# Kernel tuning notes

Measured on AMD Instinct MI355X. Metric: run time of the kernel, lower is better.

Reference implementation:

```python
import jax, jax.numpy as jnp
import numpy as np

VOCAB = 50257
D_EMB = 1024
N_NODES = 4096

def setup_inputs() -> dict:
    key = jax.random.key(0)
    k1, k2, k3 = jax.random.split(key, 3)
    x = jax.random.normal(k1, (N_NODES, D_EMB), dtype=jnp.float32)
    W = jax.random.normal(k2, (VOCAB, D_EMB), dtype=jnp.float32) * 0.02
    y = jax.random.randint(k3, (N_NODES,), 0, VOCAB, dtype=jnp.int64)
    return {"x": x, "W": W, "y": y}

def reference(x, W, y):
    # Decoder: logits = x @ W.T  -> (n_nodes, vocab)
    logits = jnp.einsum('nd,vd->nv', x, W)
    # CrossEntropyLoss (mean reduction)
    logp = jax.nn.log_softmax(logits, axis=-1)
    nll = -jnp.take_along_axis(logp, y[:, None], axis=-1)[:, 0]
    return jnp.mean(nll)
```

## Files before the change

### kernel.cpp

```cpp
#include <hip/hip_runtime.h>
#include <hip/hip_bf16.h>
#include <math.h>


#define N_NODES 4096
#define D_EMB   1024
#define VOCAB   50257
#define VPAD    50304
#define NT      393

typedef __attribute__((ext_vector_type(8))) short short8;
typedef __attribute__((ext_vector_type(4))) float f32x4;

__device__ __forceinline__ unsigned short f2bf(float f) {
  unsigned int x = __float_as_uint(f);
  x += 0x7fffu + ((x >> 16) & 1u);
  return (unsigned short)(x >> 16);
}

__global__ void cvt_w_kernel(const float* __restrict__ W, unsigned short* __restrict__ Wb) {
  long long gid = (long long)blockIdx.x * 256 + threadIdx.x;
  long long e = gid << 3;
  int row = (int)(e >> 10);
  short8 o;
  if (row < VOCAB) {
    const float4* p = (const float4*)(W + e);
    float4 u = p[0];
    float4 v = p[1];
    o[0] = (short)f2bf(u.x); o[1] = (short)f2bf(u.y); o[2] = (short)f2bf(u.z); o[3] = (short)f2bf(u.w);
    o[4] = (short)f2bf(v.x); o[5] = (short)f2bf(v.y); o[6] = (short)f2bf(v.z); o[7] = (short)f2bf(v.w);
  } else {
    o[0]=0; o[1]=0; o[2]=0; o[3]=0; o[4]=0; o[5]=0; o[6]=0; o[7]=0;
  }
  *(short8*)(Wb + e) = o;
}

__global__ void cvt_x_kernel(const float* __restrict__ x, unsigned short* __restrict__ Xb) {
  long long gid = (long long)blockIdx.x * 256 + threadIdx.x;
  long long e = gid << 3;
  const float4* p = (const float4*)(x + e);
  float4 u = p[0];
  float4 v = p[1];
  short8 o;
  o[0] = (short)f2bf(u.x); o[1] = (short)f2bf(u.y); o[2] = (short)f2bf(u.z); o[3] = (short)f2bf(u.w);
  o[4] = (short)f2bf(v.x); o[5] = (short)f2bf(v.y); o[6] = (short)f2bf(v.z); o[7] = (short)f2bf(v.w);
  *(short8*)(Xb + e) = o;
}

__global__ void dot_y_kernel(const float* __restrict__ x, const float* __restrict__ W,
                             const int* __restrict__ y, float* __restrict__ logit_y) {
  __shared__ float red[4];
  const int n = blockIdx.x;
  const int t = threadIdx.x;
  const int lbl = y[n];
  const float* xr = x + ((long long)n << 10);
  const float* wr = W + ((long long)lbl << 10);
  float s = 0.f;
  #pragma unroll
  for (int i = 0; i < 4; ++i) {
    int k = t + i * 256;
    s = fmaf(xr[k], wr[k], s);
  }
  #pragma unroll
  for (int m = 32; m; m >>= 1) s += __shfl_xor(s, m, 64);
  if ((t & 63) == 0) red[t >> 6] = s;
  __syncthreads();
  if (t == 0) logit_y[n] = red[0] + red[1] + red[2] + red[3];
}

__global__ __launch_bounds__(256) void gemm_stats_kernel(
    const unsigned short* __restrict__ Xb,
    const unsigned short* __restrict__ Wb,
    float2* __restrict__ partials)
{
  __shared__ unsigned short As[128 * 64];
  __shared__ unsigned short Bs[128 * 64];
  __shared__ float2 stats[128][2];

  const int tid  = threadIdx.x;
  const int lane = tid & 63;
  const int wid  = tid >> 6;
  const int wr   = wid >> 1;
  const int wc   = wid & 1;
  const int g    = lane >> 4;
  const int r16  = lane & 15;

  const int rowTile = blockIdx.x;
  const int vocTile = blockIdx.y;

  const long long abase = (long long)rowTile * 128 * D_EMB;
  const long long bbase = (long long)vocTile * 128 * D_EMB;

  f32x4 acc[4][4];
  #pragma unroll
  for (int m = 0; m < 4; ++m)
    #pragma unroll
    for (int n = 0; n < 4; ++n)
      #pragma unroll
      for (int j = 0; j < 4; ++j)
        acc[m][n][j] = 0.f;

  const int kk_st  = (tid & 7) << 3;
  const int row_st = tid >> 3;

  for (int k0 = 0; k0 < D_EMB; k0 += 64) {
    if (k0) __syncthreads();
    #pragma unroll
    for (int it = 0; it < 4; ++it) {
      const int idx = it * 256 + tid;
      const int row = it * 32 + row_st;
      const unsigned short* ga = Xb + abase + (long long)row * D_EMB + k0 + kk_st;
      const unsigned short* gb = Wb + bbase + (long long)row * D_EMB + k0 + kk_st;
      __builtin_amdgcn_global_load_lds((const __attribute__((address_space(1))) void*)ga,
                                       (__attribute__((address_space(3))) void*)(As + idx * 8),
                                       16, 0, 0);
      __builtin_amdgcn_global_load_lds((const __attribute__((address_space(1))) void*)gb,
                                       (__attribute__((address_space(3))) void*)(Bs + idx * 8),
                                       16, 0, 0);
    }
    __syncthreads();

    short8 a[4][2], b[4][2];
    #pragma unroll
    for (int m = 0; m < 4; ++m)
      #pragma unroll
      for (int kk = 0; kk < 2; ++kk)
        a[m][kk] = *(const short8*)(As + (wr * 64 + m * 16 + r16) * 64 + kk * 32 + g * 8);
    #pragma unroll
    for (int n = 0; n < 4; ++n)
      #pragma unroll
      for (int kk = 0; kk < 2; ++kk)
        b[n][kk] = *(const short8*)(Bs + (wc * 64 + n * 16 + r16) * 64 + kk * 32 + g * 8);

    #pragma unroll
    for (int m = 0; m < 4; ++m)
      #pragma unroll
      for (int n = 0; n < 4; ++n) {
        acc[m][n] = __builtin_amdgcn_mfma_f32_16x16x32_bf16(a[m][0], b[n][0], acc[m][n], 0, 0, 0);
        acc[m][n] = __builtin_amdgcn_mfma_f32_16x16x32_bf16(a[m][1], b[n][1], acc[m][n], 0, 0, 0);
      }
  }

  const int colbase = vocTile * 128 + wc * 64;
  #pragma unroll
  for (int m = 0; m < 4; ++m) {
    #pragma unroll
    for (int j = 0; j < 4; ++j) {
      float vmax = -INFINITY;
      #pragma unroll
      for (int n = 0; n < 4; ++n) {
        const int colg = colbase + n * 16 + r16;
        float v = (colg < VOCAB) ? acc[m][n][j] : -INFINITY;
        vmax = fmaxf(vmax, v);
      }
      vmax = fmaxf(vmax, __shfl_xor(vmax, 1));
      vmax = fmaxf(vmax, __shfl_xor(vmax, 2));
      vmax = fmaxf(vmax, __shfl_xor(vmax, 4));
      vmax = fmaxf(vmax, __shfl_xor(vmax, 8));
      float ssum = 0.f;
      #pragma unroll
      for (int n = 0; n < 4; ++n) {
        const int colg = colbase + n * 16 + r16;
        if (colg < VOCAB) ssum += __expf(acc[m][n][j] - vmax);
      }
      ssum += __shfl_xor(ssum, 1);
      ssum += __shfl_xor(ssum, 2);
      ssum += __shfl_xor(ssum, 4);
      ssum += __shfl_xor(ssum, 8);
      if (r16 == 0) {
        const int rloc = wr * 64 + m * 16 + g * 4 + j;
        stats[rloc][wc] = make_float2(vmax, ssum);
      }
    }
  }
  __syncthreads();
  if (tid < 128) {
    float2 p0 = stats[tid][0];
    float2 p1 = stats[tid][1];
    float M = fmaxf(p0.x, p1.x);
    float S = p0.y * __expf(p0.x - M) + p1.y * __expf(p1.x - M);
    partials[(long long)vocTile * N_NODES + rowTile * 128 + tid] = make_float2(M, S);
  }
}

__global__ void lse_kernel(const float2* __restrict__ partials,
                           const float* __restrict__ logit_y,
                           float* __restrict__ row_nll) {
  const int n = blockIdx.x * 256 + threadIdx.x;
  float M = -INFINITY, S = 0.f;
  for (int t = 0; t < NT; ++t) {
    float2 p = partials[(long long)t * N_NODES + n];
    float newM = fmaxf(M, p.x);
    S = S * __expf(M - newM) + p.y * __expf(p.x - newM);
    M = newM;
  }
  row_nll[n] = (M + logf(S)) - logit_y[n];
}

__global__ void mean_kernel(const float* __restrict__ row_nll, float* __restrict__ out) {
  __shared__ float red[4];
  float s = 0.f;
  for (int i = threadIdx.x; i < N_NODES; i += 256) s += row_nll[i];
  #pragma unroll
  for (int m = 32; m; m >>= 1) s += __shfl_xor(s, m, 64);
  if ((threadIdx.x & 63) == 0) red[threadIdx.x >> 6] = s;
  __syncthreads();
  if (threadIdx.x == 0) out[0] = (red[0] + red[1] + red[2] + red[3]) * (1.0f / N_NODES);
}

extern "C" void kernel_launch(void* const* d_in, const int* in_sizes, int n_in,
                              void* d_out, int out_size, void* d_ws, size_t ws_size,
                              hipStream_t stream) {
  const float* x = (const float*)d_in[0];
  const float* W = (const float*)d_in[1];
  const int*   y = (const int*)d_in[2];
  float* out = (float*)d_out;

  char* ws = (char*)d_ws;
  unsigned short* Wb = (unsigned short*)ws;
  unsigned short* Xb = (unsigned short*)(ws + 103022592);
  float2* partials   = (float2*)(ws + 111411200);
  float* logit_y     = (float*)(ws + 124289024);
  float* row_nll     = (float*)(ws + 124305408);

  hipLaunchKernelGGL(cvt_w_kernel, dim3(VPAD * (D_EMB / 8) / 256), dim3(256), 0, stream, W, Wb);
  hipLaunchKernelGGL(cvt_x_kernel, dim3(N_NODES * (D_EMB / 8) / 256), dim3(256), 0, stream, x, Xb);
  hipLaunchKernelGGL(dot_y_kernel, dim3(N_NODES), dim3(256), 0, stream, x, W, y, logit_y);
  hipLaunchKernelGGL(gemm_stats_kernel, dim3(32, NT), dim3(256), 0, stream, Xb, Wb, partials);
  hipLaunchKernelGGL(lse_kernel, dim3(N_NODES / 256), dim3(256), 0, stream, partials, logit_y, row_nll);
  hipLaunchKernelGGL(mean_kernel, dim3(1), dim3(256), 0, stream, row_nll, out);
}
```

Before: 964.2 us.

## Use 256x256 double-buffered swizzled GEMM tiles with prefetch and row-major partials

Replaces the 128x128 single-buffered GEMM with a 256x256 tile per 512-thread block. LDS is double-buffered so the next k-slice is prefetched during MFMA work, and the LDS layout is XOR-swizzled to avoid bank conflicts. MFMA sections run at raised wave priority. Partials are stored row-major so the LSE kernel can reduce each row with a full wavefront. The larger tile cuts global reloads of X and W, but it raises register and LDS pressure and adds more padding.

```diff
diff --git a/kernel.cpp b/kernel.cpp
--- a/kernel.cpp
+++ b/kernel.cpp
@@ -6,8 +6,9 @@
 #define N_NODES 4096
 #define D_EMB   1024
 #define VOCAB   50257
-#define VPAD    50304
-#define NT      393
+#define VPAD    50432
+#define NT      197
+#define KT      16
 
 typedef __attribute__((ext_vector_type(8))) short short8;
 typedef __attribute__((ext_vector_type(4))) float f32x4;
@@ -68,89 +69,162 @@
   if (t == 0) logit_y[n] = red[0] + red[1] + red[2] + red[3];
 }
 
-__global__ __launch_bounds__(256) void gemm_stats_kernel(
+#define MFMAQ(Q, AF)                                                                  \
+  do {                                                                                \
+    _Pragma("unroll")                                                                 \
+    for (int ni = 0; ni < 4; ++ni) {                                                  \
+      _Pragma("unroll")                                                               \
+      for (int kk = 0; kk < 2; ++kk) {                                                \
+        acc[2*(Q)  ][ni] = __builtin_amdgcn_mfma_f32_16x16x32_bf16(AF[0][kk], bf[ni][kk], acc[2*(Q)  ][ni], 0, 0, 0); \
+        acc[2*(Q)+1][ni] = __builtin_amdgcn_mfma_f32_16x16x32_bf16(AF[1][kk], bf[ni][kk], acc[2*(Q)+1][ni], 0, 0, 0); \
+      }                                                                               \
+    }                                                                                 \
+  } while (0)
+
+#define STAGE(U)                                                                      \
+  do {                                                                                \
+    const int _b = (U) & 1;                                                           \
+    const long long _ko = (long long)(U) * 64;                                        \
+    _Pragma("unroll")                                                                 \
+    for (int h = 0; h < 2; ++h) {                                                     \
+      _Pragma("unroll")                                                               \
+      for (int p = 0; p < 2; ++p) {                                                   \
+        __builtin_amdgcn_global_load_lds(                                             \
+            (const __attribute__((address_space(1))) void*)(Xb + abase[h][p] + _ko),  \
+            (__attribute__((address_space(3))) void*)(sh + _b*32768 + h*8192 + p*4096 + dst0), \
+            16, 0, 0);                                                                \
+      }                                                                               \
+    }                                                                                 \
+    _Pragma("unroll")                                                                 \
+    for (int h = 0; h < 2; ++h) {                                                     \
+      _Pragma("unroll")                                                               \
+      for (int p = 0; p < 2; ++p) {                                                   \
+        __builtin_amdgcn_global_load_lds(                                             \
+            (const __attribute__((address_space(1))) void*)(Wb + bbase[h][p] + _ko),  \
+            (__attribute__((address_space(3))) void*)(sh + _b*32768 + 16384 + h*8192 + p*4096 + dst0), \
+            16, 0, 0);                                                                \
+      }                                                                               \
+    }                                                                                 \
+  } while (0)
+
+__global__ __launch_bounds__(512, 2) void gemm_stats_kernel(
     const unsigned short* __restrict__ Xb,
     const unsigned short* __restrict__ Wb,
     float2* __restrict__ partials)
 {
-  __shared__ unsigned short As[128 * 64];
-  __shared__ unsigned short Bs[128 * 64];
-  __shared__ float2 stats[128][2];
+  __shared__ __align__(16) unsigned short sh[65536];
 
   const int tid  = threadIdx.x;
   const int lane = tid & 63;
   const int wid  = tid >> 6;
-  const int wr   = wid >> 1;
-  const int wc   = wid & 1;
+  const int wr   = wid >> 2;
+  const int wcol = wid & 3;
   const int g    = lane >> 4;
   const int r16  = lane & 15;
 
-  const int rowTile = blockIdx.x;
-  const int vocTile = blockIdx.y;
-
-  const long long abase = (long long)rowTile * 128 * D_EMB;
-  const long long bbase = (long long)vocTile * 128 * D_EMB;
-
-  f32x4 acc[4][4];
-  #pragma unroll
-  for (int m = 0; m < 4; ++m)
+  const int bm0 = blockIdx.x * 256;
+  const int bn0 = blockIdx.y * 256;
+
+  const int srb = tid >> 3;
+  const int scg = ((tid & 7) << 3) ^ ((srb & 7) << 3);
+  const int dst0 = tid * 8;
+  long long abase[2][2], bbase[2][2];
+  #pragma unroll
+  for (int h = 0; h < 2; ++h)
+    #pragma unroll
+    for (int p = 0; p < 2; ++p) {
+      abase[h][p] = (long long)(bm0 + h*128 + p*64 + srb) * D_EMB + scg;
+      bbase[h][p] = (long long)(bn0 + h*128 + p*64 + srb) * D_EMB + scg;
+    }
+
+  f32x4 acc[8][4];
+  #pragma unroll
+  for (int m = 0; m < 8; ++m)
     #pragma unroll
     for (int n = 0; n < 4; ++n)
       #pragma unroll
       for (int j = 0; j < 4; ++j)
         acc[m][n][j] = 0.f;
 
-  const int kk_st  = (tid & 7) << 3;
-  const int row_st = tid >> 3;
-
-  for (int k0 = 0; k0 < D_EMB; k0 += 64) {
-    if (k0) __syncthreads();
-    #pragma unroll
-    for (int it = 0; it < 4; ++it) {
-      const int idx = it * 256 + tid;
-      const int row = it * 32 + row_st;
-      const unsigned short* ga = Xb + abase + (long long)row * D_EMB + k0 + kk_st;
-      const unsigned short* gb = Wb + bbase + (long long)row * D_EMB + k0 + kk_st;
-      __builtin_amdgcn_global_load_lds((const __attribute__((address_space(1))) void*)ga,
-                                       (__attribute__((address_space(3))) void*)(As + idx * 8),
-                                       16, 0, 0);
-      __builtin_amdgcn_global_load_lds((const __attribute__((address_space(1))) void*)gb,
-                                       (__attribute__((address_space(3))) void*)(Bs + idx * 8),
-                                       16, 0, 0);
-    }
-    __syncthreads();
-
-    short8 a[4][2], b[4][2];
-    #pragma unroll
-    for (int m = 0; m < 4; ++m)
-      #pragma unroll
-      for (int kk = 0; kk < 2; ++kk)
-        a[m][kk] = *(const short8*)(As + (wr * 64 + m * 16 + r16) * 64 + kk * 32 + g * 8);
-    #pragma unroll
-    for (int n = 0; n < 4; ++n)
-      #pragma unroll
-      for (int kk = 0; kk < 2; ++kk)
-        b[n][kk] = *(const short8*)(Bs + (wc * 64 + n * 16 + r16) * 64 + kk * 32 + g * 8);
-
-    #pragma unroll
-    for (int m = 0; m < 4; ++m)
-      #pragma unroll
-      for (int n = 0; n < 4; ++n) {
-        acc[m][n] = __builtin_amdgcn_mfma_f32_16x16x32_bf16(a[m][0], b[n][0], acc[m][n], 0, 0, 0);
-        acc[m][n] = __builtin_amdgcn_mfma_f32_16x16x32_bf16(a[m][1], b[n][1], acc[m][n], 0, 0, 0);
-      }
-  }
-
-  const int colbase = vocTile * 128 + wc * 64;
-  #pragma unroll
-  for (int m = 0; m < 4; ++m) {
+  const int arow = wr * 128 + r16;
+  const int brow = wcol * 64 + r16;
+  const int sw   = (r16 & 7) << 3;
+  const int colp0 = (g * 8) ^ sw;
+  const int colp1 = (32 + g * 8) ^ sw;
+
+  STAGE(0);
+  STAGE(1);
+  asm volatile("s_waitcnt vmcnt(8)" ::: "memory");
+  __builtin_amdgcn_s_barrier();
+
+  for (int u = 0; u < KT; ++u) {
+    const unsigned short* Ab = sh + (u & 1) * 32768;
+    const unsigned short* Bb = Ab + 16384;
+
+    short8 bf[4][2], aA[2][2], aB[2][2];
+    #pragma unroll
+    for (int ni = 0; ni < 4; ++ni) {
+      bf[ni][0] = *(const short8*)(Bb + (brow + ni*16)*64 + colp0);
+      bf[ni][1] = *(const short8*)(Bb + (brow + ni*16)*64 + colp1);
+    }
+    #pragma unroll
+    for (int i = 0; i < 2; ++i) {
+      aA[i][0] = *(const short8*)(Ab + (arow + i*16)*64 + colp0);
+      aA[i][1] = *(const short8*)(Ab + (arow + i*16)*64 + colp1);
+      aB[i][0] = *(const short8*)(Ab + (arow + (2+i)*16)*64 + colp0);
+      aB[i][1] = *(const short8*)(Ab + (arow + (2+i)*16)*64 + colp1);
+    }
+
+    __builtin_amdgcn_s_setprio(1);
+    MFMAQ(0, aA);
+    __builtin_amdgcn_s_setprio(0);
+
+    #pragma unroll
+    for (int i = 0; i < 2; ++i) {
+      aA[i][0] = *(const short8*)(Ab + (arow + (4+i)*16)*64 + colp0);
+      aA[i][1] = *(const short8*)(Ab + (arow + (4+i)*16)*64 + colp1);
+    }
+    __builtin_amdgcn_s_setprio(1);
+    MFMAQ(1, aB);
+    __builtin_amdgcn_s_setprio(0);
+
+    #pragma unroll
+    for (int i = 0; i < 2; ++i) {
+      aB[i][0] = *(const short8*)(Ab + (arow + (6+i)*16)*64 + colp0);
+      aB[i][1] = *(const short8*)(Ab + (arow + (6+i)*16)*64 + colp1);
+    }
+    __builtin_amdgcn_s_setprio(1);
+    MFMAQ(2, aA);
+    __builtin_amdgcn_s_setprio(0);
+
+    asm volatile("s_waitcnt lgkmcnt(0)" ::: "memory");
+    __builtin_amdgcn_s_barrier();
+
+    if (u < KT - 2) STAGE(u + 2);
+
+    __builtin_amdgcn_s_setprio(1);
+    MFMAQ(3, aB);
+    __builtin_amdgcn_s_setprio(0);
+
+    if (u < KT - 2) {
+      asm volatile("s_waitcnt vmcnt(8)" ::: "memory");
+      __builtin_amdgcn_s_barrier();
+    } else if (u == KT - 2) {
+      asm volatile("s_waitcnt vmcnt(0)" ::: "memory");
+      __builtin_amdgcn_s_barrier();
+    }
+  }
+
+  float2 (*stats)[4] = (float2 (*)[4])sh;
+  #pragma unroll
+  for (int mi = 0; mi < 8; ++mi) {
     #pragma unroll
     for (int j = 0; j < 4; ++j) {
       float vmax = -INFINITY;
       #pragma unroll
-      for (int n = 0; n < 4; ++n) {
-        const int colg = colbase + n * 16 + r16;
-        float v = (colg < VOCAB) ? acc[m][n][j] : -INFINITY;
+      for (int ni = 0; ni < 4; ++ni) {
+        const int colg = bn0 + wcol*64 + ni*16 + r16;
+        float v = (colg < VOCAB) ? acc[mi][ni][j] : -INFINITY;
         vmax = fmaxf(vmax, v);
       }
       vmax = fmaxf(vmax, __shfl_xor(vmax, 1));
@@ -159,42 +233,51 @@
       vmax = fmaxf(vmax, __shfl_xor(vmax, 8));
       float ssum = 0.f;
       #pragma unroll
-      for (int n = 0; n < 4; ++n) {
-        const int colg = colbase + n * 16 + r16;
-        if (colg < VOCAB) ssum += __expf(acc[m][n][j] - vmax);
+      for (int ni = 0; ni < 4; ++ni) {
+        const int colg = bn0 + wcol*64 + ni*16 + r16;
+        if (colg < VOCAB) ssum += __expf(acc[mi][ni][j] - vmax);
       }
       ssum += __shfl_xor(ssum, 1);
       ssum += __shfl_xor(ssum, 2);
       ssum += __shfl_xor(ssum, 4);
       ssum += __shfl_xor(ssum, 8);
       if (r16 == 0) {
-        const int rloc = wr * 64 + m * 16 + g * 4 + j;
-        stats[rloc][wc] = make_float2(vmax, ssum);
+        stats[wr*128 + mi*16 + g*4 + j][wcol] = make_float2(vmax, ssum);
       }
     }
   }
   __syncthreads();
-  if (tid < 128) {
-    float2 p0 = stats[tid][0];
-    float2 p1 = stats[tid][1];
-    float M = fmaxf(p0.x, p1.x);
-    float S = p0.y * __expf(p0.x - M) + p1.y * __expf(p1.x - M);
-    partials[(long long)vocTile * N_NODES + rowTile * 128 + tid] = make_float2(M, S);
+  if (tid < 256) {
+    float2 a0 = stats[tid][0], a1 = stats[tid][1], a2 = stats[tid][2], a3 = stats[tid][3];
+    float M = fmaxf(fmaxf(a0.x, a1.x), fmaxf(a2.x, a3.x));
+    float S = a0.y * __expf(a0.x - M) + a1.y * __expf(a1.x - M)
+            + a2.y * __expf(a2.x - M) + a3.y * __expf(a3.x - M);
+    partials[(long long)(bm0 + tid) * NT + blockIdx.y] = make_float2(M, S);
   }
 }
 
 __global__ void lse_kernel(const float2* __restrict__ partials,
                            const float* __restrict__ logit_y,
                            float* __restrict__ row_nll) {
-  const int n = blockIdx.x * 256 + threadIdx.x;
+  const int n = blockIdx.x * 4 + (threadIdx.x >> 6);
+  const int l = threadIdx.x & 63;
+  const float2* pr = partials + (long long)n * NT;
   float M = -INFINITY, S = 0.f;
-  for (int t = 0; t < NT; ++t) {
-    float2 p = partials[(long long)t * N_NODES + n];
-    float newM = fmaxf(M, p.x);
-    S = S * __expf(M - newM) + p.y * __expf(p.x - newM);
-    M = newM;
-  }
-  row_nll[n] = (M + logf(S)) - logit_y[n];
+  for (int t = l; t < NT; t += 64) {
+    float2 p = pr[t];
+    float nM = fmaxf(M, p.x);
+    S = S * __expf(M - nM) + p.y * __expf(p.x - nM);
+    M = nM;
+  }
+  #pragma unroll
+  for (int off = 1; off < 64; off <<= 1) {
+    float Mo = __shfl_xor(M, off);
+    float So = __shfl_xor(S, off);
+    float nM = fmaxf(M, Mo);
+    S = S * __expf(M - nM) + So * __expf(Mo - nM);
+    M = nM;
+  }
+  if (l == 0) row_nll[n] = (M + logf(S)) - logit_y[n];
 }
 
 __global__ void mean_kernel(const float* __restrict__ row_nll, float* __restrict__ out) {
@@ -218,15 +301,15 @@
 
   char* ws = (char*)d_ws;
   unsigned short* Wb = (unsigned short*)ws;
-  unsigned short* Xb = (unsigned short*)(ws + 103022592);
-  float2* partials   = (float2*)(ws + 111411200);
-  float* logit_y     = (float*)(ws + 124289024);
-  float* row_nll     = (float*)(ws + 124305408);
+  unsigned short* Xb = (unsigned short*)(ws + 103284736);
+  float2* partials   = (float2*)(ws + 111673344);
+  float* logit_y     = (float*)(ws + 118128640);
+  float* row_nll     = (float*)(ws + 118145024);
 
   hipLaunchKernelGGL(cvt_w_kernel, dim3(VPAD * (D_EMB / 8) / 256), dim3(256), 0, stream, W, Wb);
   hipLaunchKernelGGL(cvt_x_kernel, dim3(N_NODES * (D_EMB / 8) / 256), dim3(256), 0, stream, x, Xb);
   hipLaunchKernelGGL(dot_y_kernel, dim3(N_NODES), dim3(256), 0, stream, x, W, y, logit_y);
-  hipLaunchKernelGGL(gemm_stats_kernel, dim3(32, NT), dim3(256), 0, stream, Xb, Wb, partials);
-  hipLaunchKernelGGL(lse_kernel, dim3(N_NODES / 256), dim3(256), 0, stream, partials, logit_y, row_nll);
+  hipLaunchKernelGGL(gemm_stats_kernel, dim3(16, NT), dim3(512), 0, stream, Xb, Wb, partials);
+  hipLaunchKernelGGL(lse_kernel, dim3(N_NODES / 4), dim3(256), 0, stream, partials, logit_y, row_nll);
   hipLaunchKernelGGL(mean_kernel, dim3(1), dim3(256), 0, stream, row_nll, out);
 }
```

Measured after the change: 803.6 us. 16.7% less time.
